# Optimization experiments

Measured on AMD Instinct MI355X. Metric: run time of the kernel, lower is better.

The kernel has to match this reference:

```python
import jax, jax.numpy as jnp
import numpy as np

B, S, D = 4, 1024, 768
NH, HD = 12, 64
E, TOP_K = 8, 2
DFF = 4 * D

def _ln(x, s, b, eps=1e-5):
    m = jnp.mean(x, axis=-1, keepdims=True)
    v = jnp.var(x, axis=-1, keepdims=True)
    return (x - m) * jax.lax.rsqrt(v + eps) * s + b

def setup_inputs() -> dict:
    key = jax.random.key(0)
    ks = jax.random.split(key, 24)
    g = lambda i, shape, sc: jax.random.normal(ks[i], shape, jnp.float32) * sc
    d = {
        'x': g(0, (B, S, D), 1.0),
        'noise': g(1, (B, S, E), 1.0),
        'wq': g(2, (D, D), 0.02), 'bq': jnp.zeros((D,), jnp.float32),
        'wk': g(3, (D, D), 0.02), 'bk': jnp.zeros((D,), jnp.float32),
        'wv': g(4, (D, D), 0.02), 'bv': jnp.zeros((D,), jnp.float32),
        'wo': g(5, (D, D), 0.02), 'bo': jnp.zeros((D,), jnp.float32),
        'ln1_s': jnp.ones((D,), jnp.float32), 'ln1_b': jnp.zeros((D,), jnp.float32),
        'ln2_s': jnp.ones((D,), jnp.float32), 'ln2_b': jnp.zeros((D,), jnp.float32),
        'r_w': g(6, (D, E), 0.02), 'r_b': jnp.zeros((E,), jnp.float32),
        'n_w': g(7, (D, E), 0.02), 'n_b': jnp.zeros((E,), jnp.float32),
        'e_w1': g(8, (E, D, DFF), 0.02), 'e_b1': jnp.zeros((E, DFF), jnp.float32),
        'e_w2': g(9, (E, DFF, D), 0.02), 'e_b2': jnp.zeros((E, D), jnp.float32),
    }
    return d

def reference(x, noise, wq, bq, wk, bk, wv, bv, wo, bo,
              ln1_s, ln1_b, ln2_s, ln2_b, r_w, r_b, n_w, n_b,
              e_w1, e_b1, e_w2, e_b2):
    # --- attention + residual ---
    h1 = _ln(x, ln1_s, ln1_b)
    q = (h1 @ wq + bq).reshape(B, S, NH, HD).transpose(0, 2, 1, 3)
    k = (h1 @ wk + bk).reshape(B, S, NH, HD).transpose(0, 2, 1, 3)
    v = (h1 @ wv + bv).reshape(B, S, NH, HD).transpose(0, 2, 1, 3)
    attn = jnp.einsum('bhqd,bhkd->bhqk', q, k) / jnp.sqrt(jnp.float32(HD))
    attn = jax.nn.softmax(attn, axis=-1)
    o = jnp.einsum('bhqk,bhkd->bhqd', attn, v)
    o = o.transpose(0, 2, 1, 3).reshape(B, S, D) @ wo + bo
    x = x + o
    # --- noisy top-k MoE + residual ---
    h2 = _ln(x, ln2_s, ln2_b)
    logits = h2 @ r_w + r_b
    nl = h2 @ n_w + n_b
    noisy = logits + noise * jax.nn.softplus(nl)  # [B,S,E]
    _, ind = jax.lax.top_k(noisy, TOP_K)          # [B,S,K]
    mask = jnp.sum(jax.nn.one_hot(ind, E, dtype=jnp.float32), axis=-2) > 0
    gate = jax.nn.softmax(jnp.where(mask, noisy, -jnp.inf), axis=-1)  # [B,S,E]
    # dense-equivalent expert compute (gate is exactly 0 for unselected experts)
    eh = jax.nn.relu(jnp.einsum('bsd,edh->ebsh', h2, e_w1) + e_b1[:, None, None, :])
    eo = jnp.einsum('ebsh,ehd->ebsd', eh, e_w2) + e_b2[:, None, None, :]
    moe = jnp.einsum('ebsd,bse->bsd', eo, gate)
    return x + moe
```

## Files before the change

kernel.cpp:

```cpp
#include <hip/hip_runtime.h>

#define DEV static __device__ __forceinline__

typedef __attribute__((ext_vector_type(8))) short v8s;
typedef __attribute__((ext_vector_type(4))) float v4f;

constexpr int Bn = 4, Sn = 1024, Dn = 768, NHn = 12, HDn = 64, En = 8, DFFn = 3072;
constexpr int Tn = Bn * Sn;
constexpr int NROWS = 2 * Tn;
constexpr int DHALF = DFFn / 2;
constexpr size_t MB = 1024 * 1024;


DEV float bf2f(unsigned short h) {
    union { unsigned int u; float f; } c; c.u = ((unsigned int)h) << 16; return c.f;
}
DEV unsigned short f2bf(float f) {
    union { float f; unsigned int u; } c; c.f = f;
    return (unsigned short)((c.u + 0x7fffu + ((c.u >> 16) & 1u)) >> 16);
}
DEV v4f mfma16(v8s a, v8s b, v4f c) {
    return __builtin_amdgcn_mfma_f32_16x16x32_bf16(a, b, c, 0, 0, 0);
}

__global__ __launch_bounds__(256) void transpose_f32(const float* __restrict__ src,
                                                     int src_ld, long src_zs,
                                                     unsigned short* __restrict__ dsthi,
                                                     unsigned short* __restrict__ dstlo,
                                                     int dst_ld, long dst_zs) {
    src += (long)blockIdx.z * src_zs;
    dsthi += (long)blockIdx.z * dst_zs;
    if (dstlo) dstlo += (long)blockIdx.z * dst_zs;
    __shared__ float tile[64][65];
    int tid = threadIdx.x, tx = blockIdx.x, ty = blockIdx.y;
    int r = tid >> 2, c0 = (tid & 3) * 16;
    const float* sp = src + (long)(ty * 64 + r) * src_ld + tx * 64 + c0;
#pragma unroll
    for (int i = 0; i < 4; ++i) {
        float4 f = *(const float4*)(sp + i * 4);
        tile[r][c0 + i * 4 + 0] = f.x;
        tile[r][c0 + i * 4 + 1] = f.y;
        tile[r][c0 + i * 4 + 2] = f.z;
        tile[r][c0 + i * 4 + 3] = f.w;
    }
    __syncthreads();
    int dl = tid >> 2, s0 = (tid & 3) * 16;
    unsigned short hh[16] __attribute__((aligned(16)));
    unsigned short ll[16] __attribute__((aligned(16)));
#pragma unroll
    for (int i = 0; i < 16; ++i) {
        float f = tile[s0 + i][dl];
        unsigned short h0 = f2bf(f);
        hh[i] = h0;
        ll[i] = f2bf(f - bf2f(h0));
    }
    long o = (long)(tx * 64 + dl) * dst_ld + ty * 64 + s0;
    *(uint4*)(dsthi + o) = ((uint4*)hh)[0];
    *(uint4*)(dsthi + o + 8) = ((uint4*)hh)[1];
    if (dstlo) {
        *(uint4*)(dstlo + o) = ((uint4*)ll)[0];
        *(uint4*)(dstlo + o + 8) = ((uint4*)ll)[1];
    }
}

__global__ __launch_bounds__(256) void ln1_split(const float* __restrict__ in_f,
                                                 const float* __restrict__ sc,
                                                 const float* __restrict__ bi,
                                                 unsigned short* __restrict__ hi,
                                                 unsigned short* __restrict__ lo) {
    int row = blockIdx.x, tid = threadIdx.x;
    long base = (long)row * Dn;
    float x[3];
#pragma unroll
    for (int j = 0; j < 3; ++j) x[j] = in_f[base + tid + j * 256];
    __shared__ float red[4];
    float s = x[0] + x[1] + x[2];
    for (int off = 32; off; off >>= 1) s += __shfl_down(s, off, 64);
    if ((tid & 63) == 0) red[tid >> 6] = s;
    __syncthreads();
    float mean = (red[0] + red[1] + red[2] + red[3]) * (1.0f / Dn);
    __syncthreads();
    float ss = 0.f;
#pragma unroll
    for (int j = 0; j < 3; ++j) { float d0 = x[j] - mean; ss += d0 * d0; }
    for (int off = 32; off; off >>= 1) ss += __shfl_down(ss, off, 64);
    if ((tid & 63) == 0) red[tid >> 6] = ss;
    __syncthreads();
    float var = (red[0] + red[1] + red[2] + red[3]) * (1.0f / Dn);
    float rstd = 1.0f / sqrtf(var + 1e-5f);
#pragma unroll
    for (int j = 0; j < 3; ++j) {
        int d = tid + j * 256;
        float y = (x[j] - mean) * rstd * sc[d] + bi[d];
        unsigned short h0 = f2bf(y);
        hi[base + d] = h0;
        lo[base + d] = f2bf(y - bf2f(h0));
    }
}

__global__ __launch_bounds__(256) void ln2_router(const float* __restrict__ in_f,
                                                  const float* __restrict__ xres,
                                                  const float* __restrict__ sc,
                                                  const float* __restrict__ bi,
                                                  const float* __restrict__ rwt,
                                                  const float* __restrict__ rb,
                                                  const float* __restrict__ nb,
                                                  const float* __restrict__ noise,
                                                  unsigned short* __restrict__ h2hi,
                                                  float* __restrict__ gates,
                                                  int* __restrict__ ind) {
    int t = blockIdx.x, tid = threadIdx.x;
    int w = tid >> 6, lane = tid & 63;
    long base = (long)t * Dn;
    float x[3];
#pragma unroll
    for (int j = 0; j < 3; ++j) x[j] = in_f[base + tid + j * 256] + xres[base + tid + j * 256];
    __shared__ float red[4];
    float s = x[0] + x[1] + x[2];
    for (int off = 32; off; off >>= 1) s += __shfl_down(s, off, 64);
    if ((tid & 63) == 0) red[tid >> 6] = s;
    __syncthreads();
    float mean = (red[0] + red[1] + red[2] + red[3]) * (1.0f / Dn);
    __syncthreads();
    float ss = 0.f;
#pragma unroll
    for (int j = 0; j < 3; ++j) { float d0 = x[j] - mean; ss += d0 * d0; }
    for (int off = 32; off; off >>= 1) ss += __shfl_down(ss, off, 64);
    if ((tid & 63) == 0) red[tid >> 6] = ss;
    __syncthreads();
    float var = (red[0] + red[1] + red[2] + red[3]) * (1.0f / Dn);
    float rstd = 1.0f / sqrtf(var + 1e-5f);
    float y[3];
#pragma unroll
    for (int j = 0; j < 3; ++j) {
        int d = tid + j * 256;
        y[j] = (x[j] - mean) * rstd * sc[d] + bi[d];
        h2hi[base + d] = f2bf(y[j]);
    }
    float acc[16];
#pragma unroll
    for (int e = 0; e < 16; ++e) {
        const float* wp = rwt + e * Dn + tid;
        acc[e] = y[0] * wp[0] + y[1] * wp[256] + y[2] * wp[512];
    }
#pragma unroll
    for (int e = 0; e < 16; ++e)
        for (int off = 32; off; off >>= 1) acc[e] += __shfl_down(acc[e], off, 64);
    __shared__ float red2[4][16];
    if (lane == 0)
#pragma unroll
        for (int e = 0; e < 16; ++e) red2[w][e] = acc[e];
    __syncthreads();
    if (tid == 0) {
        float noisy[8];
#pragma unroll
        for (int e = 0; e < 8; ++e) {
            float lg = red2[0][e] + red2[1][e] + red2[2][e] + red2[3][e] + rb[e];
            float nv = red2[0][8 + e] + red2[1][8 + e] + red2[2][8 + e] + red2[3][8 + e] + nb[e];
            float sp = fmaxf(nv, 0.f) + log1pf(expf(-fabsf(nv)));
            noisy[e] = lg + noise[(long)t * En + e] * sp;
        }
        int i0 = 0;
        for (int e = 1; e < 8; ++e) if (noisy[e] > noisy[i0]) i0 = e;
        int i1 = (i0 == 0) ? 1 : 0;
        for (int e = 0; e < 8; ++e) if (e != i0 && noisy[e] > noisy[i1]) i1 = e;
        float mm = fmaxf(noisy[i0], noisy[i1]);
        float e0 = expf(noisy[i0] - mm), e1 = expf(noisy[i1] - mm);
        float inv = 1.0f / (e0 + e1);
        gates[t] = e0 * inv;
        gates[Tn + t] = e1 * inv;
        ind[t] = i0;
        ind[Tn + t] = i1;
    }
}

__global__ __launch_bounds__(1024) void sort_rows(const int* __restrict__ ind,
                                                  int* __restrict__ meta,
                                                  int* __restrict__ rows,
                                                  int* __restrict__ pos) {
    __shared__ int wtot[8][17];
    __shared__ int bb[8];
    int tid = threadIdx.x, wv = tid >> 6, ln = tid & 63;
    int codes[8];
    int h[8] = {0, 0, 0, 0, 0, 0, 0, 0};
#pragma unroll
    for (int k = 0; k < 8; ++k) {
        int i = tid * 8 + k;
        int e = ind[(i & 1) * Tn + (i >> 1)];
        codes[k] = e;
        ++h[e];
    }
    int pre[8];
#pragma unroll
    for (int e = 0; e < 8; ++e) {
        int x = h[e];
#pragma unroll
        for (int off = 1; off < 64; off <<= 1) {
            int y = __shfl_up(x, off, 64);
            if (ln >= off) x += y;
        }
        pre[e] = x - h[e];
        if (ln == 63) wtot[e][wv] = x;
    }
    __syncthreads();
    if (tid < 8) {
        int run = 0;
        for (int w2 = 0; w2 < 16; ++w2) {
            int v = wtot[tid][w2];
            wtot[tid][w2] = run;
            run += v;
        }
        wtot[tid][16] = run;
        meta[tid] = run;
    }
    __syncthreads();
    if (tid == 0) {
        int b = 0;
        for (int e = 0; e < 8; ++e) {
            bb[e] = b;
            meta[16 + e] = b;
            b += wtot[e][16];
        }
        meta[24] = b;
    }
    __syncthreads();
    int c[8];
#pragma unroll
    for (int e = 0; e < 8; ++e) c[e] = bb[e] + wtot[e][wv] + pre[e];
#pragma unroll
    for (int k = 0; k < 8; ++k) {
        int e = codes[k];
        int code = tid * 8 + k;
        rows[c[e]] = code;
        pos[code] = c[e];
        ++c[e];
    }
}

__global__ void pack_router(const float* __restrict__ rw, const float* __restrict__ nw,
                            float* __restrict__ rwt) {
    int idx = blockIdx.x * 256 + threadIdx.x;
    int e = idx / Dn, d = idx - e * Dn;
    rwt[idx] = (e < 8) ? rw[d * En + e] : nw[d * En + (e - 8)];
}

__global__ void pack_bias(const float* __restrict__ bq, const float* __restrict__ bk,
                          const float* __restrict__ bv, float* __restrict__ bqkv) {
    int i = blockIdx.x * 256 + threadIdx.x;
    bqkv[i] = (i < 768) ? bq[i] : (i < 1536 ? bk[i - 768] : bv[i - 1536]);
}

__global__ __launch_bounds__(256, 2) void gemm_bs(
    const unsigned short* __restrict__ Ahi, const unsigned short* __restrict__ Alo,
    int lda, long za,
    const unsigned short* __restrict__ Bhi, const unsigned short* __restrict__ Blo,
    int ldb, long zb,
    const float* __restrict__ bias,
    float* __restrict__ Cf, int ldc, long zc, int K, int zdiv, int catomic, int mode,
    unsigned short* __restrict__ oqh, unsigned short* __restrict__ oql,
    unsigned short* __restrict__ okh, unsigned short* __restrict__ okl,
    unsigned short* __restrict__ ovh, unsigned short* __restrict__ ovl) {
    int z = blockIdx.z;
    int zi = z / zdiv, ks = z - zi * zdiv;
    int Klen = K / zdiv, k0base = ks * Klen;
    Ahi += (long)zi * za;
    Alo += (long)zi * za;
    Bhi += (long)zi * zb;
    Blo += (long)zi * zb;
    int n0 = blockIdx.x * 128, m0 = blockIdx.y * 128;
    int tid = threadIdx.x, w = tid >> 6, lane = tid & 63, quad = lane >> 4, l16 = lane & 15;
    int wm = w >> 1, wn = w & 1;
    __shared__ unsigned short Ah[128][40], Al[128][40], Bh[128][40], Bl[128][40];
    v4f acc[4][4] = {};
    int ar = tid >> 1, ac = (tid & 1) * 16;
    const unsigned short* pah = Ahi + (long)(m0 + ar) * lda + k0base + ac;
    const unsigned short* pal = Alo + (long)(m0 + ar) * lda + k0base + ac;
    const unsigned short* pbh = Bhi + (long)(n0 + ar) * ldb + k0base + ac;
    const unsigned short* pbl = Blo + (long)(n0 + ar) * ldb + k0base + ac;
    int nsteps = Klen >> 5;
    uint4 ra0, ra1, rb0, rb1, rc0, rc1, rd0, rd1;
#define LOADK(kt) { int o_ = (kt) << 5; \
    ra0 = *(const uint4*)(pah + o_); ra1 = *(const uint4*)(pah + o_ + 8); \
    rb0 = *(const uint4*)(pal + o_); rb1 = *(const uint4*)(pal + o_ + 8); \
    rc0 = *(const uint4*)(pbh + o_); rc1 = *(const uint4*)(pbh + o_ + 8); \
    rd0 = *(const uint4*)(pbl + o_); rd1 = *(const uint4*)(pbl + o_ + 8); }
    LOADK(0);
    for (int kt = 0; kt < nsteps; ++kt) {
        *(uint4*)&Ah[ar][ac] = ra0;
        *(uint4*)&Ah[ar][ac + 8] = ra1;
        *(uint4*)&Al[ar][ac] = rb0;
        *(uint4*)&Al[ar][ac + 8] = rb1;
        *(uint4*)&Bh[ar][ac] = rc0;
        *(uint4*)&Bh[ar][ac + 8] = rc1;
        *(uint4*)&Bl[ar][ac] = rd0;
        *(uint4*)&Bl[ar][ac + 8] = rd1;
        __syncthreads();
        if (kt + 1 < nsteps) LOADK(kt + 1);
        v8s afh[4], afl[4];
#pragma unroll
        for (int mt = 0; mt < 4; ++mt) {
            afh[mt] = *(const v8s*)&Ah[wm * 64 + mt * 16 + l16][quad * 8];
            afl[mt] = *(const v8s*)&Al[wm * 64 + mt * 16 + l16][quad * 8];
        }
#pragma unroll
        for (int nt = 0; nt < 4; ++nt) {
            v8s bbh = *(const v8s*)&Bh[wn * 64 + nt * 16 + l16][quad * 8];
            v8s bbl = *(const v8s*)&Bl[wn * 64 + nt * 16 + l16][quad * 8];
#pragma unroll
            for (int mt = 0; mt < 4; ++mt) acc[mt][nt] = mfma16(afh[mt], bbh, acc[mt][nt]);
#pragma unroll
            for (int mt = 0; mt < 4; ++mt) acc[mt][nt] = mfma16(afl[mt], bbh, acc[mt][nt]);
#pragma unroll
            for (int mt = 0; mt < 4; ++mt) acc[mt][nt] = mfma16(afh[mt], bbl, acc[mt][nt]);
        }
        __syncthreads();
    }
#undef LOADK
    if (mode == 1) {
#pragma unroll
        for (int mt = 0; mt < 4; ++mt)
#pragma unroll
            for (int nt = 0; nt < 4; ++nt)
#pragma unroll
                for (int r = 0; r < 4; ++r) {
                    int row = m0 + wm * 64 + mt * 16 + quad * 4 + r;
                    int col = n0 + wn * 64 + nt * 16 + l16;
                    float v = acc[mt][nt][r] + bias[col];
                    int seg = (col >= 1536) ? 2 : (col >= 768 ? 1 : 0);
                    int c = col - seg * 768;
                    if (seg == 0) v *= 0.125f;
                    long ci = (long)row * Dn + c;
                    unsigned short* dh = (seg == 0) ? oqh : (seg == 1 ? okh : ovh);
                    unsigned short* dl = (seg == 0) ? oql : (seg == 1 ? okl : ovl);
                    unsigned short h0 = f2bf(v);
                    dh[ci] = h0;
                    dl[ci] = f2bf(v - bf2f(h0));
                }
    } else {
        long coff = (long)zi * zc;
#pragma unroll
        for (int mt = 0; mt < 4; ++mt)
#pragma unroll
            for (int nt = 0; nt < 4; ++nt)
#pragma unroll
                for (int r = 0; r < 4; ++r) {
                    int row = m0 + wm * 64 + mt * 16 + quad * 4 + r;
                    int col = n0 + wn * 64 + nt * 16 + l16;
                    float v = acc[mt][nt][r];
                    if (ks == 0 && bias) v += bias[col];
                    long ci = coff + (long)row * ldc + col;
                    if (catomic) atomicAdd(&Cf[ci], v);
                    else Cf[ci] = v;
                }
    }
}

__global__ __launch_bounds__(256) void flash_attn(
    const unsigned short* __restrict__ qhi, const unsigned short* __restrict__ qlo,
    const unsigned short* __restrict__ khi, const unsigned short* __restrict__ klo,
    const unsigned short* __restrict__ vthi, const unsigned short* __restrict__ vtlo,
    unsigned short* __restrict__ ohi, unsigned short* __restrict__ olo) {
    int g = blockIdx.y, b = g / NHn, h = g - b * NHn;
    int m0 = blockIdx.x * 128;
    int tid = threadIdx.x, w = tid >> 6, lane = tid & 63, quad = lane >> 4, l16 = lane & 15;
    __shared__ unsigned short Kh[2][64][40], Kl[2][64][40];
    __shared__ unsigned short Vh[2][64][40], Vl[2][64][40];
    __shared__ unsigned short Ph[4][2][32][40];
    v8s qh[2][2], ql[2][2];
    long qrow0 = (long)b * Sn + m0 + w * 32;
#pragma unroll
    for (int mt = 0; mt < 2; ++mt)
#pragma unroll
        for (int kk = 0; kk < 2; ++kk) {
            long off = (qrow0 + mt * 16 + l16) * Dn + h * 64 + kk * 32 + quad * 8;
            qh[mt][kk] = *(const v8s*)(qhi + off);
            ql[mt][kk] = *(const v8s*)(qlo + off);
        }
    v4f accO[2][4] = {};
    float rs[2][4] = {};
    int srow = tid >> 3, su = tid & 7, skk = su >> 2, scu = (su & 3) * 8;
    const unsigned short* kb_h = khi + ((long)b * Sn + srow) * Dn + h * 64 + skk * 32 + scu;
    const unsigned short* kb_l = klo + ((long)b * Sn + srow) * Dn + h * 64 + skk * 32 + scu;
    const unsigned short* vb_h = vthi + ((long)g * 64 + srow) * Sn + skk * 32 + scu;
    const unsigned short* vb_l = vtlo + ((long)g * 64 + srow) * Sn + skk * 32 + scu;
    uint4 pkh0, pkh1, pkl0, pkl1, pvh0, pvh1, pvl0, pvl1;
#define LOADT(t) { long ko = (long)(t) * 64 * Dn; int vo = (t) * 64; \
    pkh0 = *(const uint4*)(kb_h + ko); pkh1 = *(const uint4*)(kb_h + ko + (long)32 * Dn); \
    pkl0 = *(const uint4*)(kb_l + ko); pkl1 = *(const uint4*)(kb_l + ko + (long)32 * Dn); \
    pvh0 = *(const uint4*)(vb_h + vo); pvh1 = *(const uint4*)(vb_h + vo + 32 * Sn); \
    pvl0 = *(const uint4*)(vb_l + vo); pvl1 = *(const uint4*)(vb_l + vo + 32 * Sn); }
    LOADT(0);
    for (int t = 0; t < 16; ++t) {
        __syncthreads();
        *(uint4*)&Kh[skk][srow][scu] = pkh0;
        *(uint4*)&Kh[skk][srow + 32][scu] = pkh1;
        *(uint4*)&Kl[skk][srow][scu] = pkl0;
        *(uint4*)&Kl[skk][srow + 32][scu] = pkl1;
        *(uint4*)&Vh[skk][srow][scu] = pvh0;
        *(uint4*)&Vh[skk][srow + 32][scu] = pvh1;
        *(uint4*)&Vl[skk][srow][scu] = pvl0;
        *(uint4*)&Vl[skk][srow + 32][scu] = pvl1;
        __syncthreads();
        if (t < 15) LOADT(t + 1);
        v4f accS[2][4] = {};
#pragma unroll
        for (int nt = 0; nt < 4; ++nt)
#pragma unroll
            for (int kk = 0; kk < 2; ++kk) {
                v8s bh = *(const v8s*)&Kh[kk][nt * 16 + l16][quad * 8];
                v8s bl = *(const v8s*)&Kl[kk][nt * 16 + l16][quad * 8];
#pragma unroll
                for (int mt = 0; mt < 2; ++mt) {
                    accS[mt][nt] = mfma16(qh[mt][kk], bh, accS[mt][nt]);
                    accS[mt][nt] = mfma16(ql[mt][kk], bh, accS[mt][nt]);
                    accS[mt][nt] = mfma16(qh[mt][kk], bl, accS[mt][nt]);
                }
            }
#pragma unroll
        for (int mt = 0; mt < 2; ++mt)
#pragma unroll
            for (int r = 0; r < 4; ++r) {
                int prow = mt * 16 + quad * 4 + r;
                float psum = 0.f;
#pragma unroll
                for (int nt = 0; nt < 4; ++nt) {
                    float p = __expf(accS[mt][nt][r]);
                    unsigned short hh = f2bf(p);
                    psum += bf2f(hh);
                    Ph[w][nt >> 1][prow][(nt & 1) * 16 + l16] = hh;
                }
                rs[mt][r] += psum;
            }
#pragma unroll
        for (int kk = 0; kk < 2; ++kk) {
            v8s pa0 = *(const v8s*)&Ph[w][kk][l16][quad * 8];
            v8s pa1 = *(const v8s*)&Ph[w][kk][16 + l16][quad * 8];
#pragma unroll
            for (int nt = 0; nt < 4; ++nt) {
                v8s vh = *(const v8s*)&Vh[kk][nt * 16 + l16][quad * 8];
                v8s vl = *(const v8s*)&Vl[kk][nt * 16 + l16][quad * 8];
                accO[0][nt] = mfma16(pa0, vh, accO[0][nt]);
                accO[1][nt] = mfma16(pa1, vh, accO[1][nt]);
                accO[0][nt] = mfma16(pa0, vl, accO[0][nt]);
                accO[1][nt] = mfma16(pa1, vl, accO[1][nt]);
            }
        }
    }
#undef LOADT
#pragma unroll
    for (int mt = 0; mt < 2; ++mt)
#pragma unroll
        for (int r = 0; r < 4; ++r) {
            float s = rs[mt][r];
#pragma unroll
            for (int off = 1; off < 16; off <<= 1) s += __shfl_xor(s, off, 64);
            float inv = 1.0f / s;
            long orow = qrow0 + mt * 16 + quad * 4 + r;
#pragma unroll
            for (int nt = 0; nt < 4; ++nt) {
                float v = accO[mt][nt][r] * inv;
                unsigned short hh = f2bf(v);
                long oi = orow * Dn + h * 64 + nt * 16 + l16;
                ohi[oi] = hh;
                olo[oi] = f2bf(v - bf2f(hh));
            }
        }
}

__global__ __launch_bounds__(256) void vtrans16(const unsigned short* __restrict__ vhi,
                                                const unsigned short* __restrict__ vlo,
                                                unsigned short* __restrict__ vthi,
                                                unsigned short* __restrict__ vtlo) {
    int g = blockIdx.z, b = g / NHn, h = g % NHn;
    int stile = blockIdx.x, tid = threadIdx.x;
    __shared__ unsigned short th[64][66], tl[64][66];
    int sl = tid >> 2, c0 = (tid & 3) * 16;
    long src = (long)(b * Sn + stile * 64 + sl) * Dn + h * 64 + c0;
    *(uint4*)&th[sl][c0] = *(const uint4*)(vhi + src);
    *(uint4*)&th[sl][c0 + 8] = *(const uint4*)(vhi + src + 8);
    *(uint4*)&tl[sl][c0] = *(const uint4*)(vlo + src);
    *(uint4*)&tl[sl][c0 + 8] = *(const uint4*)(vlo + src + 8);
    __syncthreads();
    int dl = tid >> 2, s0 = (tid & 3) * 16;
    unsigned short hh[16] __attribute__((aligned(16)));
    unsigned short ll[16] __attribute__((aligned(16)));
#pragma unroll
    for (int i = 0; i < 16; ++i) {
        hh[i] = th[s0 + i][dl];
        ll[i] = tl[s0 + i][dl];
    }
    long o = (long)(g * 64 + dl) * Sn + stile * 64 + s0;
    *(uint4*)(vthi + o) = ((uint4*)hh)[0];
    *(uint4*)(vthi + o + 8) = ((uint4*)hh)[1];
    *(uint4*)(vtlo + o) = ((uint4*)ll)[0];
    *(uint4*)(vtlo + o + 8) = ((uint4*)ll)[1];
}

__global__ __launch_bounds__(256, 2) void moe_gemm1(const unsigned short* __restrict__ h2hi,
                                                    const unsigned short* __restrict__ W1t,
                                                    const float* __restrict__ eb1,
                                                    const int* __restrict__ rows,
                                                    const int* __restrict__ meta,
                                                    unsigned short* __restrict__ eh,
                                                    int half) {
    int e = blockIdx.z;
    int cnt = meta[e];
    int mb = blockIdx.y * 128;
    if (mb >= cnt) return;
    int base_e = meta[16 + e];
    int valid = cnt - mb; if (valid > 128) valid = 128;
    int tid = threadIdx.x;
    __shared__ int toks[128];
    if (tid < 128) {
        int idx = mb + tid;
        toks[tid] = rows[base_e + (idx < cnt ? idx : 0)];
    }
    __shared__ unsigned short As[128][40], Bs[128][40];
    int w = tid >> 6, lane = tid & 63, quad = lane >> 4, l16 = lane & 15;
    int wm = w >> 1, wn = w & 1;
    v4f acc[4][4] = {};
    int ar = tid >> 1, ac = (tid & 1) * 16;
    int nb0 = blockIdx.x * 128;
    const unsigned short* Wb = W1t + (long)e * DHALF * Dn;
    __syncthreads();
    const unsigned short* apg = h2hi + (long)(toks[ar] >> 1) * Dn + ac;
    const unsigned short* bpg = Wb + (long)(nb0 + ar) * Dn + ac;
    uint4 a0, a1, b0, b1;
#define LOADK(kt) { int o_ = (kt) * 32; \
    a0 = *(const uint4*)(apg + o_); a1 = *(const uint4*)(apg + o_ + 8); \
    b0 = *(const uint4*)(bpg + o_); b1 = *(const uint4*)(bpg + o_ + 8); }
    LOADK(0);
    for (int kt = 0; kt < Dn / 32; ++kt) {
        *(uint4*)&As[ar][ac] = a0;
        *(uint4*)&As[ar][ac + 8] = a1;
        *(uint4*)&Bs[ar][ac] = b0;
        *(uint4*)&Bs[ar][ac + 8] = b1;
        __syncthreads();
        if (kt + 1 < Dn / 32) LOADK(kt + 1);
        v8s af[4];
#pragma unroll
        for (int mt = 0; mt < 4; ++mt) af[mt] = *(const v8s*)&As[wm * 64 + mt * 16 + l16][quad * 8];
#pragma unroll
        for (int nt = 0; nt < 4; ++nt) {
            v8s bb = *(const v8s*)&Bs[wn * 64 + nt * 16 + l16][quad * 8];
#pragma unroll
            for (int mt = 0; mt < 4; ++mt) acc[mt][nt] = mfma16(af[mt], bb, acc[mt][nt]);
        }
        __syncthreads();
    }
#undef LOADK
#pragma unroll
    for (int mt = 0; mt < 4; ++mt)
#pragma unroll
        for (int nt = 0; nt < 4; ++nt)
#pragma unroll
            for (int r = 0; r < 4; ++r) {
                int rl = wm * 64 + mt * 16 + quad * 4 + r;
                if (rl < valid) {
                    int col = nb0 + wn * 64 + nt * 16 + l16;
                    float v = acc[mt][nt][r] + eb1[e * DFFn + half * DHALF + col];
                    v = fmaxf(v, 0.f);
                    eh[(long)(base_e + mb + rl) * DHALF + col] = f2bf(v);
                }
            }
}

__global__ __launch_bounds__(256, 2) void moe_gemm2(const unsigned short* __restrict__ eh,
                                                    const unsigned short* __restrict__ W2t,
                                                    const float* __restrict__ eb2,
                                                    const int* __restrict__ meta,
                                                    unsigned short* __restrict__ eo0,
                                                    unsigned short* __restrict__ eo1,
                                                    int accum) {
    int z = blockIdx.z;
    int e = z >> 1, ks = z & 1;
    int k0b = ks * (DHALF / 2);
    int cnt = meta[e];
    int mb = blockIdx.y * 128;
    if (mb >= cnt) return;
    int base_e = meta[16 + e];
    int valid = cnt - mb; if (valid > 128) valid = 128;
    int tid = threadIdx.x;
    __shared__ unsigned short As[128][40], Bs[128][40];
    int w = tid >> 6, lane = tid & 63, quad = lane >> 4, l16 = lane & 15;
    int wm = w >> 1, wn = w & 1;
    v4f acc[4][4] = {};
    int ar = tid >> 1, ac = (tid & 1) * 16;
    int nb0 = blockIdx.x * 128;
    const unsigned short* Wb = W2t + (long)e * Dn * DHALF;
    long arow = (long)base_e + mb + ar;
    if (arow > NROWS - 1) arow = NROWS - 1;
    const unsigned short* apg = eh + arow * DHALF + k0b + ac;
    const unsigned short* bpg = Wb + (long)(nb0 + ar) * DHALF + k0b + ac;
    uint4 a0, a1, b0, b1;
#define LOADK(kt) { int o_ = (kt) * 32; \
    a0 = *(const uint4*)(apg + o_); a1 = *(const uint4*)(apg + o_ + 8); \
    b0 = *(const uint4*)(bpg + o_); b1 = *(const uint4*)(bpg + o_ + 8); }
    LOADK(0);
    constexpr int NK = (DHALF / 2) / 32;
    for (int kt = 0; kt < NK; ++kt) {
        *(uint4*)&As[ar][ac] = a0;
        *(uint4*)&As[ar][ac + 8] = a1;
        *(uint4*)&Bs[ar][ac] = b0;
        *(uint4*)&Bs[ar][ac + 8] = b1;
        __syncthreads();
        if (kt + 1 < NK) LOADK(kt + 1);
        v8s af[4];
#pragma unroll
        for (int mt = 0; mt < 4; ++mt) af[mt] = *(const v8s*)&As[wm * 64 + mt * 16 + l16][quad * 8];
#pragma unroll
        for (int nt = 0; nt < 4; ++nt) {
            v8s bb = *(const v8s*)&Bs[wn * 64 + nt * 16 + l16][quad * 8];
#pragma unroll
            for (int mt = 0; mt < 4; ++mt) acc[mt][nt] = mfma16(af[mt], bb, acc[mt][nt]);
        }
        __syncthreads();
    }
#undef LOADK
    unsigned short* eo = ks ? eo1 : eo0;
#pragma unroll
    for (int mt = 0; mt < 4; ++mt)
#pragma unroll
        for (int nt = 0; nt < 4; ++nt)
#pragma unroll
            for (int r = 0; r < 4; ++r) {
                int rl = wm * 64 + mt * 16 + quad * 4 + r;
                if (rl < valid) {
                    int col = nb0 + wn * 64 + nt * 16 + l16;
                    long idx = (long)(base_e + mb + rl) * Dn + col;
                    float v = acc[mt][nt][r];
                    if (eb2 && ks == 0) v += eb2[e * Dn + col];
                    if (accum) v += bf2f(eo[idx]);
                    eo[idx] = f2bf(v);
                }
            }
}

__global__ __launch_bounds__(256) void final_add(const float* __restrict__ x2f,
                                                 const float* __restrict__ xres,
                                                 const unsigned short* __restrict__ eo0,
                                                 const unsigned short* __restrict__ eo1,
                                                 const float* __restrict__ gates,
                                                 const int* __restrict__ pos,
                                                 float* __restrict__ out) {
    int t = blockIdx.x, tid = threadIdx.x;
    int p0 = pos[2 * t], p1 = pos[2 * t + 1];
    float g0 = gates[t], g1 = gates[Tn + t];
    long b0 = (long)p0 * Dn, b1 = (long)p1 * Dn;
    long xb = (long)t * Dn;
#pragma unroll
    for (int j = 0; j < 3; ++j) {
        int d = tid + j * 256;
        float m0 = bf2f(eo0[b0 + d]) + bf2f(eo1[b0 + d]);
        float m1 = bf2f(eo0[b1 + d]) + bf2f(eo1[b1 + d]);
        out[xb + d] = x2f[xb + d] + xres[xb + d] + g0 * m0 + g1 * m1;
    }
}

extern "C" void kernel_launch(void* const* d_in, const int* in_sizes, int n_in,
                              void* d_out, int out_size, void* d_ws, size_t ws_size,
                              hipStream_t stream) {
    const float* x     = (const float*)d_in[0];
    const float* noise = (const float*)d_in[1];
    const float* wq = (const float*)d_in[2];
    const float* bq = (const float*)d_in[3];
    const float* wk = (const float*)d_in[4];
    const float* bk = (const float*)d_in[5];
    const float* wv = (const float*)d_in[6];
    const float* bv = (const float*)d_in[7];
    const float* wo = (const float*)d_in[8];
    const float* bo = (const float*)d_in[9];
    const float* ln1_s = (const float*)d_in[10];
    const float* ln1_b = (const float*)d_in[11];
    const float* ln2_s = (const float*)d_in[12];
    const float* ln2_b = (const float*)d_in[13];
    const float* r_w = (const float*)d_in[14];
    const float* r_b = (const float*)d_in[15];
    const float* n_w = (const float*)d_in[16];
    const float* n_b = (const float*)d_in[17];
    const float* e_w1 = (const float*)d_in[18];
    const float* e_b1 = (const float*)d_in[19];
    const float* e_w2 = (const float*)d_in[20];
    const float* e_b2 = (const float*)d_in[21];

    char* ws = (char*)d_ws;
    unsigned short* qhi  = (unsigned short*)(ws + 0);
    unsigned short* qlo  = (unsigned short*)(ws + 6 * MB);
    unsigned short* ohi  = qhi;
    unsigned short* olo  = qlo;
    unsigned short* eo1  = (unsigned short*)(ws + 0);
    unsigned short* h1hi = (unsigned short*)(ws + 12 * MB);
    unsigned short* h1lo = (unsigned short*)(ws + 18 * MB);
    unsigned short* eh   = (unsigned short*)(ws + 12 * MB);
    unsigned short* khi  = (unsigned short*)(ws + 24 * MB);
    unsigned short* klo  = (unsigned short*)(ws + 30 * MB);
    unsigned short* eo0  = (unsigned short*)(ws + 36 * MB);
    unsigned short* vhi  = (unsigned short*)(ws + 48 * MB);
    unsigned short* vlo  = (unsigned short*)(ws + 54 * MB);
    float* x2f  = (float*)(ws + 48 * MB);
    unsigned short* whalf = (unsigned short*)(ws + 60 * MB);
    unsigned short* vthi = (unsigned short*)(ws + 72 * MB);
    unsigned short* vtlo = (unsigned short*)(ws + 78 * MB);
    unsigned short* h2hi  = (unsigned short*)(ws + 78 * MB);
    unsigned short* wqkvTh = (unsigned short*)(ws + 84 * MB);
    unsigned short* wqkvTl = wqkvTh + (size_t)3 * Dn * Dn;
    unsigned short* woTh = wqkvTl + (size_t)3 * Dn * Dn;
    unsigned short* woTl = woTh + (size_t)Dn * Dn;
    char* misc = (char*)(woTl + (size_t)Dn * Dn);
    float* bqkv = (float*)misc;
    float* rwt  = (float*)(misc + 2304 * 4);
    float* gates = (float*)(misc + 2304 * 4 + 12288 * 4);
    int* ind  = (int*)((char*)gates + 2 * Tn * 4);
    int* meta = (int*)((char*)ind + 2 * Tn * 4);
    int* rows = (int*)((char*)meta + 256);
    int* pos  = rows + NROWS;

    dim3 blk(256);
    transpose_f32<<<dim3(12, 12, 1), blk, 0, stream>>>(wq, Dn, 0, wqkvTh, wqkvTl, Dn, 0);
    transpose_f32<<<dim3(12, 12, 1), blk, 0, stream>>>(wk, Dn, 0,
        wqkvTh + (size_t)Dn * Dn, wqkvTl + (size_t)Dn * Dn, Dn, 0);
    transpose_f32<<<dim3(12, 12, 1), blk, 0, stream>>>(wv, Dn, 0,
        wqkvTh + (size_t)2 * Dn * Dn, wqkvTl + (size_t)2 * Dn * Dn, Dn, 0);
    transpose_f32<<<dim3(12, 12, 1), blk, 0, stream>>>(wo, Dn, 0, woTh, woTl, Dn, 0);
    pack_bias<<<dim3(9), blk, 0, stream>>>(bq, bk, bv, bqkv);
    pack_router<<<dim3(48), blk, 0, stream>>>(r_w, n_w, rwt);
    ln1_split<<<dim3(Tn), blk, 0, stream>>>(x, ln1_s, ln1_b, h1hi, h1lo);
    gemm_bs<<<dim3(18, 32, 1), blk, 0, stream>>>(h1hi, h1lo, Dn, 0, wqkvTh, wqkvTl, Dn, 0,
        bqkv, nullptr, 0, 0, Dn, 1, 0, 1, qhi, qlo, khi, klo, vhi, vlo);
    vtrans16<<<dim3(16, 1, 48), blk, 0, stream>>>(vhi, vlo, vthi, vtlo);
    flash_attn<<<dim3(8, 48), blk, 0, stream>>>(qhi, qlo, khi, klo, vthi, vtlo, ohi, olo);
    gemm_bs<<<dim3(6, 32, 1), blk, 0, stream>>>(ohi, olo, Dn, 0, woTh, woTl, Dn, 0,
        bo, x2f, Dn, 0, Dn, 1, 0, 0, nullptr, nullptr, nullptr, nullptr, nullptr, nullptr);
    ln2_router<<<dim3(Tn), blk, 0, stream>>>(x2f, x, ln2_s, ln2_b, rwt, r_b, n_b, noise,
                                             h2hi, gates, ind);
    sort_rows<<<dim3(1), dim3(1024), 0, stream>>>(ind, meta, rows, pos);
    for (int h = 0; h < 2; ++h) {
        transpose_f32<<<dim3(24, 12, 8), blk, 0, stream>>>(
            e_w1 + (size_t)h * DHALF, DFFn, (long)Dn * DFFn, whalf, nullptr, Dn, (long)DHALF * Dn);
        moe_gemm1<<<dim3(12, 32, 8), blk, 0, stream>>>(h2hi, whalf, e_b1, rows, meta, eh, h);
        transpose_f32<<<dim3(12, 24, 8), blk, 0, stream>>>(
            e_w2 + (size_t)h * DHALF * Dn, Dn, (long)DFFn * Dn, whalf, nullptr, DHALF, (long)Dn * DHALF);
        moe_gemm2<<<dim3(6, 32, 16), blk, 0, stream>>>(eh, whalf, h == 0 ? e_b2 : nullptr,
                                                       meta, eo0, eo1, h);
    }
    final_add<<<dim3(Tn), blk, 0, stream>>>(x2f, x, eo0, eo1, gates, pos, (float*)d_out);
}
```

Baseline: 700.7 us.

## Compact MoE grouped-GEMM grid over used row tiles with XCD-aware remap

sort_rows now records the cumulative count of 128-row tiles per expert. The MoE GEMMs launch a flattened grid of at most 72 row tiles instead of 32 per expert, and map each block to its expert and tile through that prefix. This removes the many empty blocks that used to launch and exit early. The linear block id is also permuted across the 8 dies (l&7), so that blocks sharing weight tiles land together. The cost is a few extra metadata loads and a small expert search per block.

```diff
diff --git a/kernel.cpp b/kernel.cpp
--- a/kernel.cpp
+++ b/kernel.cpp
@@ -9,6 +9,7 @@
 constexpr int Tn = Bn * Sn;
 constexpr int NROWS = 2 * Tn;
 constexpr int DHALF = DFFn / 2;
+constexpr int YT = 72;
 constexpr size_t MB = 1024 * 1024;
 
 
@@ -215,13 +216,16 @@
     }
     __syncthreads();
     if (tid == 0) {
-        int b = 0;
+        int b = 0, ct = 0;
         for (int e = 0; e < 8; ++e) {
             bb[e] = b;
             meta[16 + e] = b;
             b += wtot[e][16];
+            meta[32 + e] = ct;
+            ct += (wtot[e][16] + 127) >> 7;
         }
         meta[24] = b;
+        meta[40] = ct;
     }
     __syncthreads();
     int c[8];
@@ -503,10 +507,16 @@
                                                     const int* __restrict__ meta,
                                                     unsigned short* __restrict__ eh,
                                                     int half) {
-    int e = blockIdx.z;
+    int l = blockIdx.x + 12 * blockIdx.y;
+    constexpr int L1 = 12 * YT;
+    int nl = (l & 7) * (L1 >> 3) + (l >> 3);
+    int vy = nl / 12, vx = nl - vy * 12;
+    if (vy >= meta[40]) return;
+    int e = 0;
+#pragma unroll
+    for (int i = 1; i < 8; ++i) if (meta[32 + i] <= vy) e = i;
+    int mb = (vy - meta[32 + e]) * 128;
     int cnt = meta[e];
-    int mb = blockIdx.y * 128;
-    if (mb >= cnt) return;
     int base_e = meta[16 + e];
     int valid = cnt - mb; if (valid > 128) valid = 128;
     int tid = threadIdx.x;
@@ -520,7 +530,7 @@
     int wm = w >> 1, wn = w & 1;
     v4f acc[4][4] = {};
     int ar = tid >> 1, ac = (tid & 1) * 16;
-    int nb0 = blockIdx.x * 128;
+    int nb0 = vx * 128;
     const unsigned short* Wb = W1t + (long)e * DHALF * Dn;
     __syncthreads();
     const unsigned short* apg = h2hi + (long)(toks[ar] >> 1) * Dn + ac;
@@ -572,12 +582,18 @@
                                                     unsigned short* __restrict__ eo0,
                                                     unsigned short* __restrict__ eo1,
                                                     int accum) {
-    int z = blockIdx.z;
-    int e = z >> 1, ks = z & 1;
+    int ks = blockIdx.z;
     int k0b = ks * (DHALF / 2);
+    int l = blockIdx.x + 6 * blockIdx.y;
+    constexpr int L2 = 6 * YT;
+    int nl = (l & 7) * (L2 >> 3) + (l >> 3);
+    int vy = nl / 6, vx = nl - vy * 6;
+    if (vy >= meta[40]) return;
+    int e = 0;
+#pragma unroll
+    for (int i = 1; i < 8; ++i) if (meta[32 + i] <= vy) e = i;
+    int mb = (vy - meta[32 + e]) * 128;
     int cnt = meta[e];
-    int mb = blockIdx.y * 128;
-    if (mb >= cnt) return;
     int base_e = meta[16 + e];
     int valid = cnt - mb; if (valid > 128) valid = 128;
     int tid = threadIdx.x;
@@ -586,7 +602,7 @@
     int wm = w >> 1, wn = w & 1;
     v4f acc[4][4] = {};
     int ar = tid >> 1, ac = (tid & 1) * 16;
-    int nb0 = blockIdx.x * 128;
+    int nb0 = vx * 128;
     const unsigned short* Wb = W2t + (long)e * Dn * DHALF;
     long arow = (long)base_e + mb + ar;
     if (arow > NROWS - 1) arow = NROWS - 1;
@@ -737,11 +753,11 @@
     for (int h = 0; h < 2; ++h) {
         transpose_f32<<<dim3(24, 12, 8), blk, 0, stream>>>(
             e_w1 + (size_t)h * DHALF, DFFn, (long)Dn * DFFn, whalf, nullptr, Dn, (long)DHALF * Dn);
-        moe_gemm1<<<dim3(12, 32, 8), blk, 0, stream>>>(h2hi, whalf, e_b1, rows, meta, eh, h);
+        moe_gemm1<<<dim3(12, YT, 1), blk, 0, stream>>>(h2hi, whalf, e_b1, rows, meta, eh, h);
         transpose_f32<<<dim3(12, 24, 8), blk, 0, stream>>>(
             e_w2 + (size_t)h * DHALF * Dn, Dn, (long)DFFn * Dn, whalf, nullptr, DHALF, (long)Dn * DHALF);
-        moe_gemm2<<<dim3(6, 32, 16), blk, 0, stream>>>(eh, whalf, h == 0 ? e_b2 : nullptr,
-                                                       meta, eo0, eo1, h);
+        moe_gemm2<<<dim3(6, YT, 2), blk, 0, stream>>>(eh, whalf, h == 0 ? e_b2 : nullptr,
+                                                      meta, eo0, eo1, h);
     }
     final_add<<<dim3(Tn), blk, 0, stream>>>(x2f, x, eo0, eo1, gates, pos, (float*)d_out);
 }
```

Result: faster. 655.8 us (-6.4%).
